# Performance work log

Hardware: AMD Instinct MI355X
Metric: run time of the kernel (lower is better)

The kernel has to match this reference:

```python
import jax, jax.numpy as jnp
import numpy as np

WIN = 8
SHIFT = 4
HEADS = 6

def _rel_pos_index(w):
    coords = np.stack(np.meshgrid(np.arange(w), np.arange(w), indexing='ij'))  # (2,w,w)
    cf = coords.reshape(2, -1)
    rel = (cf[:, :, None] - cf[:, None, :]).transpose(1, 2, 0)  # (N,N,2)
    rel[:, :, 0] += w - 1
    rel[:, :, 1] += w - 1
    rel[:, :, 0] *= 2 * w - 1
    return rel.sum(-1)  # (N,N) int

def _attn_mask(H, W, w, s):
    img = np.zeros((H, W))
    slices = (slice(0, -w), slice(-w, -s), slice(-s, None))
    cnt = 0
    for hs in slices:
        for ws in slices:
            img[hs, ws] = cnt
            cnt += 1
    mw = img.reshape(H // w, w, W // w, w).transpose(0, 2, 1, 3).reshape(-1, w * w)  # (nW,N)
    am = mw[:, None, :] - mw[:, :, None]
    return np.where(am != 0, -100.0, 0.0).astype(np.float32)  # (nW,N,N)

def _ln(z, g, b):
    mu = z.mean(-1, keepdims=True)
    var = z.var(-1, keepdims=True)
    return (z - mu) / jnp.sqrt(var + 1e-5) * g + b

def setup_inputs() -> dict:
    key = jax.random.key(0)
    ks = jax.random.split(key, 8)
    C, HID = 192, 768
    sc = lambda fan: 1.0 / np.sqrt(fan)
    return {
        'x': jax.random.normal(ks[0], (4, 256, 256, C), jnp.float32),
        'qkv_w': jax.random.normal(ks[1], (3 * C, C), jnp.float32) * sc(C),
        'qkv_b': jnp.zeros((3 * C,), jnp.float32),
        'proj_w': jax.random.normal(ks[2], (C, C), jnp.float32) * sc(C),
        'proj_b': jnp.zeros((C,), jnp.float32),
        'rpb': jax.random.normal(ks[3], (225, HEADS), jnp.float32) * 0.02,
        'n1_w': jnp.ones((C,), jnp.float32),
        'n1_b': jnp.zeros((C,), jnp.float32),
        'n2_w': jnp.ones((C,), jnp.float32),
        'n2_b': jnp.zeros((C,), jnp.float32),
        'fc1_w': jax.random.normal(ks[4], (HID, C), jnp.float32) * sc(C),
        'fc1_b': jnp.zeros((HID,), jnp.float32),
        'fc2_w': jax.random.normal(ks[5], (C, HID), jnp.float32) * sc(HID),
        'fc2_b': jnp.zeros((C,), jnp.float32),
    }

def reference(x, qkv_w, qkv_b, proj_w, proj_b, rpb, n1_w, n1_b, n2_w, n2_b, fc1_w, fc1_b, fc2_w, fc2_b):
    B, H, W, C = x.shape
    N = WIN * WIN
    hd = C // HEADS
    scale = hd ** -0.5

    shortcut = x.reshape(B, H * W, C)
    z = _ln(shortcut, n1_w, n1_b).reshape(B, H, W, C)
    z = jnp.roll(z, (-SHIFT, -SHIFT), axis=(1, 2))

    # window partition -> (B*nW, N, C)
    xw = z.reshape(B, H // WIN, WIN, W // WIN, WIN, C).transpose(0, 1, 3, 2, 4, 5).reshape(-1, N, C)
    B_ = xw.shape[0]

    qkv = (xw @ qkv_w.T + qkv_b).reshape(B_, N, 3, HEADS, hd).transpose(2, 0, 3, 1, 4)
    q, k, v = qkv[0] * scale, qkv[1], qkv[2]
    attn = jnp.einsum('bhnd,bhmd->bhnm', q, k)  # (B_,H,N,N)

    idx = _rel_pos_index(WIN)
    bias = rpb[idx.reshape(-1)].reshape(N, N, HEADS).transpose(2, 0, 1)  # (H,N,N)
    attn = attn + bias[None]

    mask = jnp.asarray(_attn_mask(H, W, WIN, SHIFT))  # (nW,N,N)
    nW = mask.shape[0]
    attn = attn.reshape(B_ // nW, nW, HEADS, N, N) + mask[None, :, None]
    attn = jax.nn.softmax(attn, axis=-1).reshape(B_, HEADS, N, N)

    out = jnp.einsum('bhnm,bhmd->bhnd', attn, v).transpose(0, 2, 1, 3).reshape(B_, N, C)
    out = out @ proj_w.T + proj_b

    # window reverse
    out = out.reshape(B, H // WIN, W // WIN, WIN, WIN, C).transpose(0, 1, 3, 2, 4, 5).reshape(B, H, W, C)
    out = jnp.roll(out, (SHIFT, SHIFT), axis=(1, 2)).reshape(B, H * W, C)

    h = shortcut + out
    m = _ln(h, n2_w, n2_b)
    m = jax.nn.gelu(m @ fc1_w.T + fc1_b, approximate=False)
    m = m @ fc2_w.T + fc2_b
    return (h + m).reshape(B, H, W, C)
```

## Files before the change

kernel.cpp:

```cpp
#include <hip/hip_runtime.h>
#include <hip/hip_bf16.h>

typedef __attribute__((ext_vector_type(8))) __bf16 bf16x8;
typedef __attribute__((ext_vector_type(4))) float f32x4;
typedef __hip_bfloat16 bf16;

#define SCALE_Q 0.17677669529663687f

__device__ inline float gelu_f(float x) {
  const float ax = fabsf(x) * 0.70710678118654752f;
  const float t = __builtin_amdgcn_rcpf(__builtin_fmaf(0.3275911f, ax, 1.0f));
  const float poly = t * __builtin_fmaf(t, __builtin_fmaf(t, __builtin_fmaf(t,
                     __builtin_fmaf(t, 1.061405429f, -1.453152027f),
                     1.421413741f), -0.284496736f), 0.254829592f);
  const float er = __builtin_fmaf(-poly, __expf(-ax * ax), 1.0f);
  return 0.5f * x * (1.0f + copysignf(er, x));
}

template<int K, int KC>
__global__ void cvt_frag_kernel(const float* __restrict__ in, bf16* __restrict__ out, int total) {
  int i = blockIdx.x * 256 + threadIdx.x;
  if (i < total) {
    const int n = i / K, k = i - n * K;
    out[((n >> 4) * KC + (k >> 5)) * 512 + ((k >> 3) & 3) * 128 + (n & 15) * 8 + (k & 7)] =
        __float2bfloat16(in[i]);
  }
}

__global__ __launch_bounds__(512, 2) void win_attn(const float* __restrict__ x,
                                                   const float* __restrict__ n1w,
                                                   const float* __restrict__ n1b,
                                                   const bf16* __restrict__ qwt,
                                                   const float* __restrict__ qb,
                                                   const float* __restrict__ rpb,
                                                   const bf16* __restrict__ pwt,
                                                   const float* __restrict__ pb,
                                                   float* __restrict__ hbuf) {
  __shared__ __align__(16) char smem[119072];
  char* Qt = smem;
  char* Kt = smem + 30720;
  char* Vtb = smem + 61440;
  char* Ab = smem + 89088;
  float* rpl = (float*)(smem + 113664);

  const int tid = threadIdx.x;
  const int blk = blockIdx.x;
  const long m0 = (long)blk * 64;
  const int lane = tid & 63, wid = tid >> 6;
  const int lg = lane >> 4, lr = lane & 15;

  for (int t = tid; t < 1350; t += 512) {
    const int hh = t / 225, tt = t - hh * 225;
    rpl[hh * 225 + tt] = rpb[tt * 6 + hh];
  }

  #pragma unroll
  for (int t8 = 0; t8 < 8; t8++) {
    const int row = wid * 8 + t8;
    const long t = m0 + row;
    const int b_ = (int)(t >> 6), n = (int)(t & 63);
    const int b = b_ >> 10, wk = b_ & 1023, wi = wk >> 5, wj = wk & 31;
    const int hf = (wi * 8 + (n >> 3) + 4) & 255, wf = (wj * 8 + (n & 7) + 4) & 255;
    const long g = (((long)b * 256 + hf) * 256 + wf) * 192;
    const float x0 = x[g + lane], x1 = x[g + 64 + lane], x2 = x[g + 128 + lane];
    float s = x0 + x1 + x2;
    float s2 = x0 * x0 + x1 * x1 + x2 * x2;
    #pragma unroll
    for (int msk = 1; msk < 64; msk <<= 1) { s += __shfl_xor(s, msk); s2 += __shfl_xor(s2, msk); }
    const float mu = s * (1.0f / 192.0f);
    const float rstd = rsqrtf(s2 * (1.0f / 192.0f) - mu * mu + 1e-5f);
    #pragma unroll
    for (int p = 0; p < 3; p++) {
      const int ch = p * 64 + lane;
      const float xv = (p == 0) ? x0 : (p == 1) ? x1 : x2;
      const float v = (xv - mu) * rstd * n1w[ch] + n1b[ch];
      const int c = (ch >> 3) & 7;
      const int slot = c ^ (row & 7);
      *(unsigned short*)(Ab + p * 8192 + row * 128 + slot * 16 + (ch & 7) * 2) =
          __builtin_bit_cast(unsigned short, __float2bfloat16(v));
    }
  }
  __syncthreads();

  {
    const int wrr = (wid >> 2) * 32;
    const int wcg = wid & 3;
    f32x4 acc[2][9];
    #pragma unroll
    for (int i = 0; i < 2; i++)
      #pragma unroll
      for (int j = 0; j < 9; j++) acc[i][j] = (f32x4){0.f, 0.f, 0.f, 0.f};
    const int c16base = wcg * 9;
    #pragma unroll
    for (int kc = 0; kc < 6; kc++) {
      const int q = kc >> 1;
      const int kk = (kc & 1) * 4 + lg;
      bf16x8 af[2], bfr[9];
      #pragma unroll
      for (int i = 0; i < 2; i++) {
        const int row = wrr + i * 16 + lr;
        af[i] = *(const bf16x8*)(Ab + q * 8192 + row * 128 + ((kk ^ (row & 7)) * 16));
      }
      #pragma unroll
      for (int j = 0; j < 9; j++)
        bfr[j] = *(const bf16x8*)(qwt + ((c16base + j) * 6 + kc) * 512 + lane * 8);
      #pragma unroll
      for (int i = 0; i < 2; i++)
        #pragma unroll
        for (int j = 0; j < 9; j++)
          acc[i][j] = __builtin_amdgcn_mfma_f32_16x16x32_bf16(af[i], bfr[j], acc[i][j], 0, 0, 0);
    }
    __syncthreads();
    #pragma unroll
    for (int i = 0; i < 2; i++) {
      #pragma unroll
      for (int j = 0; j < 9; j++) {
        #pragma unroll
        for (int r = 0; r < 4; r++) {
          const int n = wrr + i * 16 + lg * 4 + r;
          const int cn = wcg * 144 + j * 16 + lr;
          float v = acc[i][j][r] + qb[cn];
          const int which = cn / 192, rem = cn - which * 192, head = rem >> 5, d = rem & 31;
          unsigned short us;
          if (which == 0) { v *= SCALE_Q; us = __builtin_bit_cast(unsigned short, __float2bfloat16(v));
            *(unsigned short*)(Qt + head * 5120 + n * 80 + d * 2) = us; }
          else if (which == 1) { us = __builtin_bit_cast(unsigned short, __float2bfloat16(v));
            *(unsigned short*)(Kt + head * 5120 + n * 80 + d * 2) = us; }
          else { us = __builtin_bit_cast(unsigned short, __float2bfloat16(v));
            *(unsigned short*)(Vtb + head * 4608 + (d * 72 + n) * 2) = us; }
        }
      }
    }
  }
  __syncthreads();

  const f32x4 z4 = {0.f, 0.f, 0.f, 0.f};
  f32x4 s[4][4];
  const int head = wid;
  if (wid < 6) {
    bf16x8 a[4], b[4];
    #pragma unroll
    for (int fi = 0; fi < 4; fi++)
      a[fi] = *(const bf16x8*)(Qt + head * 5120 + (fi * 16 + lr) * 80 + lg * 16);
    #pragma unroll
    for (int fj = 0; fj < 4; fj++)
      b[fj] = *(const bf16x8*)(Kt + head * 5120 + (fj * 16 + lr) * 80 + lg * 16);
    #pragma unroll
    for (int fi = 0; fi < 4; fi++)
      #pragma unroll
      for (int fj = 0; fj < 4; fj++)
        s[fi][fj] = __builtin_amdgcn_mfma_f32_16x16x32_bf16(a[fi], b[fj], z4, 0, 0, 0);
  }
  __syncthreads();

  bf16* P = (bf16*)(smem + head * 9216);
  if (wid < 6) {
    const int wk = blk & 1023; const int wi = wk >> 5, wj = wk & 31;
    const bool eh = (wi == 31), ew = (wj == 31);
    const float* rps = rpl + head * 225;
    #pragma unroll
    for (int fi = 0; fi < 4; fi++) {
      #pragma unroll
      for (int r = 0; r < 4; r++) {
        const int n = fi * 16 + lg * 4 + r;
        const int i1 = n >> 3, j1 = n & 7;
        const int labn = (eh ? (i1 < 4 ? 3 : 6) : 0) + (ew ? (j1 < 4 ? 1 : 2) : 0);
        float vals[4];
        #pragma unroll
        for (int fj = 0; fj < 4; fj++) {
          const int m = fj * 16 + lr;
          const int i2 = m >> 3, j2 = m & 7;
          const int labm = (eh ? (i2 < 4 ? 3 : 6) : 0) + (ew ? (j2 < 4 ? 1 : 2) : 0);
          vals[fj] = s[fi][fj][r] + rps[(i1 - i2 + 7) * 15 + (j1 - j2 + 7)]
                   + (labn != labm ? -100.0f : 0.0f);
        }
        float mx = fmaxf(fmaxf(vals[0], vals[1]), fmaxf(vals[2], vals[3]));
        #pragma unroll
        for (int msk = 1; msk < 16; msk <<= 1) mx = fmaxf(mx, __shfl_xor(mx, msk));
        float pe[4]; float sum = 0.f;
        #pragma unroll
        for (int fj = 0; fj < 4; fj++) { pe[fj] = __expf(vals[fj] - mx); sum += pe[fj]; }
        #pragma unroll
        for (int msk = 1; msk < 16; msk <<= 1) sum += __shfl_xor(sum, msk);
        const float rinv = 1.0f / sum;
        #pragma unroll
        for (int fj = 0; fj < 4; fj++)
          P[n * 72 + fj * 16 + lr] = __float2bfloat16(pe[fj] * rinv);
      }
    }
  }
  __syncthreads();

  if (wid < 6) {
    f32x4 o[4][2];
    #pragma unroll
    for (int fi = 0; fi < 4; fi++)
      #pragma unroll
      for (int fd = 0; fd < 2; fd++) o[fi][fd] = z4;
    const bf16* vt = (const bf16*)(Vtb + head * 4608);
    #pragma unroll
    for (int ks = 0; ks < 2; ks++) {
      bf16x8 pa[4], vb[2];
      #pragma unroll
      for (int fi = 0; fi < 4; fi++)
        pa[fi] = *(const bf16x8*)(P + (fi * 16 + lr) * 72 + ks * 32 + lg * 8);
      #pragma unroll
      for (int fd = 0; fd < 2; fd++)
        vb[fd] = *(const bf16x8*)(vt + (fd * 16 + lr) * 72 + ks * 32 + lg * 8);
      #pragma unroll
      for (int fi = 0; fi < 4; fi++)
        #pragma unroll
        for (int fd = 0; fd < 2; fd++)
          o[fi][fd] = __builtin_amdgcn_mfma_f32_16x16x32_bf16(pa[fi], vb[fd], o[fi][fd], 0, 0, 0);
    }
    #pragma unroll
    for (int fi = 0; fi < 4; fi++)
      #pragma unroll
      for (int fd = 0; fd < 2; fd++)
        #pragma unroll
        for (int r = 0; r < 4; r++) {
          const int n = fi * 16 + lg * 4 + r;
          const int ch = head * 32 + fd * 16 + lr;
          const int p = ch >> 6, c = (ch >> 3) & 7;
          const int slot = c ^ (n & 7);
          *(unsigned short*)(Ab + p * 8192 + n * 128 + slot * 16 + (ch & 7) * 2) =
              __builtin_bit_cast(unsigned short, __float2bfloat16(o[fi][fd][r]));
        }
  }
  __syncthreads();

  {
    const int wrr2 = (wid >> 2) * 32, wcg2 = wid & 3;
    f32x4 accp[2][3];
    #pragma unroll
    for (int i = 0; i < 2; i++)
      #pragma unroll
      for (int j = 0; j < 3; j++) accp[i][j] = (f32x4){0.f, 0.f, 0.f, 0.f};
    #pragma unroll
    for (int kc = 0; kc < 6; kc++) {
      const int q = kc >> 1;
      const int kk = (kc & 1) * 4 + lg;
      bf16x8 af[2], bfr[3];
      #pragma unroll
      for (int i = 0; i < 2; i++) {
        const int row = wrr2 + i * 16 + lr;
        af[i] = *(const bf16x8*)(Ab + q * 8192 + row * 128 + ((kk ^ (row & 7)) * 16));
      }
      #pragma unroll
      for (int j = 0; j < 3; j++)
        bfr[j] = *(const bf16x8*)(pwt + ((wcg2 * 3 + j) * 6 + kc) * 512 + lane * 8);
      #pragma unroll
      for (int i = 0; i < 2; i++)
        #pragma unroll
        for (int j = 0; j < 3; j++)
          accp[i][j] = __builtin_amdgcn_mfma_f32_16x16x32_bf16(af[i], bfr[j], accp[i][j], 0, 0, 0);
    }
    #pragma unroll
    for (int i = 0; i < 2; i++) {
      #pragma unroll
      for (int j = 0; j < 3; j++) {
        #pragma unroll
        for (int r = 0; r < 4; r++) {
          const long m = m0 + wrr2 + i * 16 + lg * 4 + r;
          const int cn = wcg2 * 48 + j * 16 + lr;
          const float v = accp[i][j][r] + pb[cn];
          const long b_ = m >> 6; const int n = (int)(m & 63);
          const int b = (int)(b_ >> 10), wk = (int)(b_ & 1023), wi = wk >> 5, wj = wk & 31;
          const int i_ = n >> 3, j_ = n & 7;
          const int hf = (wi * 8 + i_ + 4) & 255, wf = (wj * 8 + j_ + 4) & 255;
          const long g = (((long)b * 256 + hf) * 256 + wf) * 192 + cn;
          hbuf[g] = x[g] + v;
        }
      }
    }
  }
}

__global__ __launch_bounds__(512, 2) void mlp_fused(const float* __restrict__ hbuf,
                                                    const float* __restrict__ n2w,
                                                    const float* __restrict__ n2b,
                                                    const bf16* __restrict__ w1t,
                                                    const float* __restrict__ b1,
                                                    const bf16* __restrict__ w2t,
                                                    const float* __restrict__ b2,
                                                    float* __restrict__ outp) {
  __shared__ __align__(16) char smem[122880];
  char* Ab = smem;
  char* G  = smem + 24576;

  const int tid = threadIdx.x;
  const long m0 = (long)blockIdx.x * 64;
  const int lane = tid & 63, wid = tid >> 6;
  const int lg = lane >> 4, lr = lane & 15;

  #pragma unroll
  for (int t8 = 0; t8 < 8; t8++) {
    const int row = wid * 8 + t8;
    const long g = (m0 + row) * 192;
    const float x0 = hbuf[g + lane], x1 = hbuf[g + 64 + lane], x2 = hbuf[g + 128 + lane];
    float s = x0 + x1 + x2;
    float s2 = x0 * x0 + x1 * x1 + x2 * x2;
    #pragma unroll
    for (int msk = 1; msk < 64; msk <<= 1) { s += __shfl_xor(s, msk); s2 += __shfl_xor(s2, msk); }
    const float mu = s * (1.0f / 192.0f);
    const float rstd = rsqrtf(s2 * (1.0f / 192.0f) - mu * mu + 1e-5f);
    #pragma unroll
    for (int p = 0; p < 3; p++) {
      const int ch = p * 64 + lane;
      const float xv = (p == 0) ? x0 : (p == 1) ? x1 : x2;
      const float v = (xv - mu) * rstd * n2w[ch] + n2b[ch];
      const int c = (ch >> 3) & 7;
      const int slot = c ^ (row & 7);
      *(unsigned short*)(Ab + p * 8192 + row * 128 + slot * 16 + (ch & 7) * 2) =
          __builtin_bit_cast(unsigned short, __float2bfloat16(v));
    }
  }
  __syncthreads();

  f32x4 acc1[4][6];
  #pragma unroll
  for (int i = 0; i < 4; i++)
    #pragma unroll
    for (int j = 0; j < 6; j++) acc1[i][j] = (f32x4){0.f, 0.f, 0.f, 0.f};

  const int c16base = wid * 6;
  #pragma unroll
  for (int kc = 0; kc < 6; kc++) {
    const int q = kc >> 1;
    const int kk = (kc & 1) * 4 + lg;
    bf16x8 af[4], bfr[6];
    #pragma unroll
    for (int i = 0; i < 4; i++) {
      const int row = i * 16 + lr;
      af[i] = *(const bf16x8*)(Ab + q * 8192 + row * 128 + ((kk ^ (row & 7)) * 16));
    }
    #pragma unroll
    for (int j = 0; j < 6; j++)
      bfr[j] = *(const bf16x8*)(w1t + ((c16base + j) * 6 + kc) * 512 + lane * 8);
    #pragma unroll
    for (int i = 0; i < 4; i++)
      #pragma unroll
      for (int j = 0; j < 6; j++)
        acc1[i][j] = __builtin_amdgcn_mfma_f32_16x16x32_bf16(af[i], bfr[j], acc1[i][j], 0, 0, 0);
  }

  #pragma unroll
  for (int j = 0; j < 6; j++) {
    const int n = wid * 96 + j * 16 + lr;
    const float bj = b1[n];
    const int c = n >> 3;
    #pragma unroll
    for (int i = 0; i < 4; i++) {
      #pragma unroll
      for (int r = 0; r < 4; r++) {
        const int m = i * 16 + lg * 4 + r;
        const int slot = (c & ~7) | ((c & 7) ^ (m & 7));
        *(unsigned short*)(G + m * 1536 + slot * 16 + (n & 7) * 2) =
            __builtin_bit_cast(unsigned short, __float2bfloat16(gelu_f(acc1[i][j][r] + bj)));
      }
    }
  }
  __syncthreads();

  const int wt = wid >> 2, wn = wid & 3;
  f32x4 acc2[2][3];
  #pragma unroll
  for (int i = 0; i < 2; i++)
    #pragma unroll
    for (int j = 0; j < 3; j++) acc2[i][j] = (f32x4){0.f, 0.f, 0.f, 0.f};

  for (int kt = 0; kt < 24; kt++) {
    const int c2 = kt * 4 + lg;
    bf16x8 af2[2], bfr2[3];
    #pragma unroll
    for (int i = 0; i < 2; i++) {
      const int grow = wt * 32 + i * 16 + lr;
      const int slot2 = (c2 & ~7) | ((c2 & 7) ^ (grow & 7));
      af2[i] = *(const bf16x8*)(G + grow * 1536 + slot2 * 16);
    }
    #pragma unroll
    for (int j = 0; j < 3; j++)
      bfr2[j] = *(const bf16x8*)(w2t + ((wn * 3 + j) * 24 + kt) * 512 + lane * 8);
    #pragma unroll
    for (int i = 0; i < 2; i++)
      #pragma unroll
      for (int j = 0; j < 3; j++)
        acc2[i][j] = __builtin_amdgcn_mfma_f32_16x16x32_bf16(af2[i], bfr2[j], acc2[i][j], 0, 0, 0);
  }

  #pragma unroll
  for (int j = 0; j < 3; j++) {
    const int cn = wn * 48 + j * 16 + lr;
    const float bj = b2[cn];
    #pragma unroll
    for (int i = 0; i < 2; i++) {
      #pragma unroll
      for (int r = 0; r < 4; r++) {
        const long m = m0 + wt * 32 + i * 16 + lg * 4 + r;
        outp[m * 192 + cn] = acc2[i][j][r] + bj + hbuf[m * 192 + cn];
      }
    }
  }
}

extern "C" void kernel_launch(void* const* d_in, const int* in_sizes, int n_in,
                              void* d_out, int out_size, void* d_ws, size_t ws_size,
                              hipStream_t stream) {
  const float* x      = (const float*)d_in[0];
  const float* qkv_w  = (const float*)d_in[1];
  const float* qkv_b  = (const float*)d_in[2];
  const float* proj_w = (const float*)d_in[3];
  const float* proj_b = (const float*)d_in[4];
  const float* rpb    = (const float*)d_in[5];
  const float* n1_w   = (const float*)d_in[6];
  const float* n1_b   = (const float*)d_in[7];
  const float* n2_w   = (const float*)d_in[8];
  const float* n2_b   = (const float*)d_in[9];
  const float* fc1_w  = (const float*)d_in[10];
  const float* fc1_b  = (const float*)d_in[11];
  const float* fc2_w  = (const float*)d_in[12];
  const float* fc2_b  = (const float*)d_in[13];

  char* ws = (char*)d_ws;
  bf16* qkvw_t  = (bf16*)(ws);
  bf16* projw_t = (bf16*)(ws + 221184);
  bf16* fc1w_t  = (bf16*)(ws + 294912);
  bf16* fc2w_t  = (bf16*)(ws + 589824);
  float* hbuf   = (float*)(ws + (1L << 20));

  cvt_frag_kernel<192, 6><<<432, 256, 0, stream>>>(qkv_w, qkvw_t, 110592);
  cvt_frag_kernel<192, 6><<<144, 256, 0, stream>>>(proj_w, projw_t, 36864);
  cvt_frag_kernel<192, 6><<<576, 256, 0, stream>>>(fc1_w, fc1w_t, 147456);
  cvt_frag_kernel<768, 24><<<576, 256, 0, stream>>>(fc2_w, fc2w_t, 147456);

  win_attn<<<4096, 512, 0, stream>>>(x, n1_w, n1_b, qkvw_t, qkv_b, rpb, projw_t, proj_b, hbuf);
  mlp_fused<<<4096, 512, 0, stream>>>(hbuf, n2_w, n2_b, fc1w_t, fc1_b, fc2w_t, fc2_b,
                                      (float*)d_out);
}
```

Measured before the change: 802.1 us.

## Shrink window-attention LDS footprint with aliased swizzled buffers for higher occupancy

```diff
diff --git a/kernel.cpp b/kernel.cpp
--- a/kernel.cpp
+++ b/kernel.cpp
@@ -27,7 +27,7 @@
   }
 }
 
-__global__ __launch_bounds__(512, 2) void win_attn(const float* __restrict__ x,
+__global__ __launch_bounds__(512, 4) void win_attn(const float* __restrict__ x,
                                                    const float* __restrict__ n1w,
                                                    const float* __restrict__ n1b,
                                                    const bf16* __restrict__ qwt,
@@ -36,12 +36,10 @@
                                                    const bf16* __restrict__ pwt,
                                                    const float* __restrict__ pb,
                                                    float* __restrict__ hbuf) {
-  __shared__ __align__(16) char smem[119072];
-  char* Qt = smem;
-  char* Kt = smem + 30720;
-  char* Vtb = smem + 61440;
-  char* Ab = smem + 89088;
-  float* rpl = (float*)(smem + 113664);
+  __shared__ __align__(16) char smem[79136];
+  char* QK = smem;
+  char* VA = smem + 49152;
+  float* rpl = (float*)(smem + 73728);
 
   const int tid = threadIdx.x;
   const int blk = blockIdx.x;
@@ -76,7 +74,7 @@
       const float v = (xv - mu) * rstd * n1w[ch] + n1b[ch];
       const int c = (ch >> 3) & 7;
       const int slot = c ^ (row & 7);
-      *(unsigned short*)(Ab + p * 8192 + row * 128 + slot * 16 + (ch & 7) * 2) =
+      *(unsigned short*)(VA + p * 8192 + row * 128 + slot * 16 + (ch & 7) * 2) =
           __builtin_bit_cast(unsigned short, __float2bfloat16(v));
     }
   }
@@ -99,7 +97,7 @@
       #pragma unroll
       for (int i = 0; i < 2; i++) {
         const int row = wrr + i * 16 + lr;
-        af[i] = *(const bf16x8*)(Ab + q * 8192 + row * 128 + ((kk ^ (row & 7)) * 16));
+        af[i] = *(const bf16x8*)(VA + q * 8192 + row * 128 + ((kk ^ (row & 7)) * 16));
       }
       #pragma unroll
       for (int j = 0; j < 9; j++)
@@ -122,12 +120,19 @@
           float v = acc[i][j][r] + qb[cn];
           const int which = cn / 192, rem = cn - which * 192, head = rem >> 5, d = rem & 31;
           unsigned short us;
-          if (which == 0) { v *= SCALE_Q; us = __builtin_bit_cast(unsigned short, __float2bfloat16(v));
-            *(unsigned short*)(Qt + head * 5120 + n * 80 + d * 2) = us; }
-          else if (which == 1) { us = __builtin_bit_cast(unsigned short, __float2bfloat16(v));
-            *(unsigned short*)(Kt + head * 5120 + n * 80 + d * 2) = us; }
-          else { us = __builtin_bit_cast(unsigned short, __float2bfloat16(v));
-            *(unsigned short*)(Vtb + head * 4608 + (d * 72 + n) * 2) = us; }
+          if (which == 0) {
+            v *= SCALE_Q; us = __builtin_bit_cast(unsigned short, __float2bfloat16(v));
+            const int c = d >> 3, slot = c ^ (n & 3);
+            *(unsigned short*)(QK + head * 8192 + n * 64 + slot * 16 + (d & 7) * 2) = us;
+          } else if (which == 1) {
+            us = __builtin_bit_cast(unsigned short, __float2bfloat16(v));
+            const int c = d >> 3, slot = c ^ (n & 3);
+            *(unsigned short*)(QK + head * 8192 + 4096 + n * 64 + slot * 16 + (d & 7) * 2) = us;
+          } else {
+            us = __builtin_bit_cast(unsigned short, __float2bfloat16(v));
+            const int c = n >> 3, slot = c ^ (d & 7);
+            *(unsigned short*)(VA + head * 4096 + d * 128 + slot * 16 + (n & 7) * 2) = us;
+          }
         }
       }
     }
@@ -140,11 +145,15 @@
   if (wid < 6) {
     bf16x8 a[4], b[4];
     #pragma unroll
-    for (int fi = 0; fi < 4; fi++)
-      a[fi] = *(const bf16x8*)(Qt + head * 5120 + (fi * 16 + lr) * 80 + lg * 16);
-    #pragma unroll
-    for (int fj = 0; fj < 4; fj++)
-      b[fj] = *(const bf16x8*)(Kt + head * 5120 + (fj * 16 + lr) * 80 + lg * 16);
+    for (int fi = 0; fi < 4; fi++) {
+      const int row = fi * 16 + lr;
+      a[fi] = *(const bf16x8*)(QK + head * 8192 + row * 64 + ((lg ^ (row & 3)) * 16));
+    }
+    #pragma unroll
+    for (int fj = 0; fj < 4; fj++) {
+      const int row = fj * 16 + lr;
+      b[fj] = *(const bf16x8*)(QK + head * 8192 + 4096 + row * 64 + ((lg ^ (row & 3)) * 16));
+    }
     #pragma unroll
     for (int fi = 0; fi < 4; fi++)
       #pragma unroll
@@ -153,7 +162,7 @@
   }
   __syncthreads();
 
-  bf16* P = (bf16*)(smem + head * 9216);
+  char* P = QK + head * 8192;
   if (wid < 6) {
     const int wk = blk & 1023; const int wi = wk >> 5, wj = wk & 31;
     const bool eh = (wi == 31), ew = (wj == 31);
@@ -184,35 +193,47 @@
         for (int msk = 1; msk < 16; msk <<= 1) sum += __shfl_xor(sum, msk);
         const float rinv = 1.0f / sum;
         #pragma unroll
-        for (int fj = 0; fj < 4; fj++)
-          P[n * 72 + fj * 16 + lr] = __float2bfloat16(pe[fj] * rinv);
-      }
-    }
-  }
-  __syncthreads();
-
+        for (int fj = 0; fj < 4; fj++) {
+          const int m = fj * 16 + lr;
+          const int c = m >> 3, slot = c ^ (n & 7);
+          *(unsigned short*)(P + n * 128 + slot * 16 + (m & 7) * 2) =
+              __builtin_bit_cast(unsigned short, __float2bfloat16(pe[fj] * rinv));
+        }
+      }
+    }
+  }
+  __syncthreads();
+
+  f32x4 o[4][2];
   if (wid < 6) {
-    f32x4 o[4][2];
     #pragma unroll
     for (int fi = 0; fi < 4; fi++)
       #pragma unroll
       for (int fd = 0; fd < 2; fd++) o[fi][fd] = z4;
-    const bf16* vt = (const bf16*)(Vtb + head * 4608);
     #pragma unroll
     for (int ks = 0; ks < 2; ks++) {
+      const int c2 = ks * 4 + lg;
       bf16x8 pa[4], vb[2];
       #pragma unroll
-      for (int fi = 0; fi < 4; fi++)
-        pa[fi] = *(const bf16x8*)(P + (fi * 16 + lr) * 72 + ks * 32 + lg * 8);
-      #pragma unroll
-      for (int fd = 0; fd < 2; fd++)
-        vb[fd] = *(const bf16x8*)(vt + (fd * 16 + lr) * 72 + ks * 32 + lg * 8);
+      for (int fi = 0; fi < 4; fi++) {
+        const int row = fi * 16 + lr;
+        pa[fi] = *(const bf16x8*)(P + row * 128 + ((c2 ^ (row & 7)) * 16));
+      }
+      #pragma unroll
+      for (int fd = 0; fd < 2; fd++) {
+        const int row = fd * 16 + lr;
+        vb[fd] = *(const bf16x8*)(VA + head * 4096 + row * 128 + ((c2 ^ (row & 7)) * 16));
+      }
       #pragma unroll
       for (int fi = 0; fi < 4; fi++)
         #pragma unroll
         for (int fd = 0; fd < 2; fd++)
           o[fi][fd] = __builtin_amdgcn_mfma_f32_16x16x32_bf16(pa[fi], vb[fd], o[fi][fd], 0, 0, 0);
     }
+  }
+  __syncthreads();
+
+  if (wid < 6) {
     #pragma unroll
     for (int fi = 0; fi < 4; fi++)
       #pragma unroll
@@ -223,7 +244,7 @@
           const int ch = head * 32 + fd * 16 + lr;
           const int p = ch >> 6, c = (ch >> 3) & 7;
           const int slot = c ^ (n & 7);
-          *(unsigned short*)(Ab + p * 8192 + n * 128 + slot * 16 + (ch & 7) * 2) =
+          *(unsigned short*)(VA + p * 8192 + n * 128 + slot * 16 + (ch & 7) * 2) =
               __builtin_bit_cast(unsigned short, __float2bfloat16(o[fi][fd][r]));
         }
   }
@@ -244,7 +265,7 @@
       #pragma unroll
       for (int i = 0; i < 2; i++) {
         const int row = wrr2 + i * 16 + lr;
-        af[i] = *(const bf16x8*)(Ab + q * 8192 + row * 128 + ((kk ^ (row & 7)) * 16));
+        af[i] = *(const bf16x8*)(VA + q * 8192 + row * 128 + ((kk ^ (row & 7)) * 16));
       }
       #pragma unroll
       for (int j = 0; j < 3; j++)
```

New measurement: 810.3 us. Within noise of the previous version (+1.0%).
